# Performance work log

Measured on AMD Instinct MI355X. Metric: run time of the kernel, lower is better.

The kernel has to match this reference:

```python
import jax, jax.numpy as jnp
import numpy as np

NEAR, FAR, N_SAMPLES = 0.5, 2.5, 64


def setup_inputs() -> dict:
    key = jax.random.key(0)
    ks = jax.random.split(key, 12)
    N = 4096
    W = 256  # MLP width
    inp = {
        "rays_o": jax.random.normal(ks[0], (N, 3), jnp.float32),
        "rays_d": jax.random.normal(ks[1], (N, 3), jnp.float32),
        "t_rand": jax.random.uniform(ks[2], (N, N_SAMPLES), jnp.float32),
        "W1": jax.random.normal(ks[3], (3, W), jnp.float32) * 0.5,
        "b1": jnp.zeros((W,), jnp.float32),
        "W2": jax.random.normal(ks[4], (W, W), jnp.float32) * (1.0 / np.sqrt(W)),
        "b2": jnp.zeros((W,), jnp.float32),
        "W3": jax.random.normal(ks[5], (W, W), jnp.float32) * (1.0 / np.sqrt(W)),
        "b3": jnp.zeros((W,), jnp.float32),
        "Wd": jax.random.normal(ks[6], (W, 1), jnp.float32) * (1.0 / np.sqrt(W)),
        "bd": jnp.zeros((1,), jnp.float32),
        "W4": jax.random.normal(ks[7], (W + 3, 128), jnp.float32) * (1.0 / np.sqrt(W + 3)),
        "b4": jnp.zeros((128,), jnp.float32),
        "W5": jax.random.normal(ks[8], (128, 3), jnp.float32) * (1.0 / np.sqrt(128)),
        "b5": jnp.zeros((3,), jnp.float32),
    }
    return inp


def _nerf_mlp(pts, viewdirs, W1, b1, W2, b2, W3, b3, Wd, bd, W4, b4, W5, b5):
    # pts, viewdirs: [N, S, 3] -> rgb [N, S, 3], density [N, S]
    h = jax.nn.relu(pts @ W1 + b1)
    h = jax.nn.relu(h @ W2 + b2)
    h = jax.nn.relu(h @ W3 + b3)
    density = (h @ Wd + bd)[..., 0]
    h2 = jax.nn.relu(jnp.concatenate([h, viewdirs], axis=-1) @ W4 + b4)
    rgb = jax.nn.sigmoid(h2 @ W5 + b5)
    return rgb, density


def reference(rays_o, rays_d, t_rand, W1, b1, W2, b2, W3, b3, Wd, bd, W4, b4, W5, b5):
    N = rays_o.shape[0]
    # Stratified sampling along rays
    t_vals = jnp.linspace(0.0, 1.0, N_SAMPLES, dtype=jnp.float32)
    z = NEAR * (1.0 - t_vals) + FAR * t_vals                      # [S]
    z_vals = jnp.broadcast_to(z, (N, N_SAMPLES))
    mids = 0.5 * (z_vals[:, 1:] + z_vals[:, :-1])
    upper = jnp.concatenate([mids, z_vals[:, -1:]], axis=-1)
    lower = jnp.concatenate([z_vals[:, :1], mids], axis=-1)
    z_vals = lower + (upper - lower) * t_rand                      # [N, S]

    pts = rays_o[:, None, :] + rays_d[:, None, :] * z_vals[..., None]  # [N, S, 3]
    viewdirs = rays_d / (jnp.linalg.norm(rays_d, axis=-1, keepdims=True) + 1e-8)
    vdirs = jnp.broadcast_to(viewdirs[:, None, :], pts.shape)

    rgb, density = _nerf_mlp(pts, vdirs, W1, b1, W2, b2, W3, b3, Wd, bd, W4, b4, W5, b5)

    # Alpha compositing
    dists = z_vals[:, 1:] - z_vals[:, :-1]
    dists = jnp.concatenate([dists, jnp.full_like(dists[:, :1], 1e10)], axis=-1)
    alpha = 1.0 - jnp.exp(-jax.nn.relu(density) * dists)           # [N, S]
    trans = jnp.cumprod(
        jnp.concatenate([jnp.ones_like(alpha[:, :1]), 1.0 - alpha[:, :-1] + 1e-10], axis=-1),
        axis=-1,
    )
    weights = alpha * trans                                        # [N, S]
    rgb_map = jnp.sum(weights[..., None] * rgb, axis=-2)           # [N, 3]
    depth_map = jnp.sum(weights * z_vals, axis=-1)                 # [N]
    acc_map = jnp.sum(weights, axis=-1)                            # [N]
    rgb_map = rgb_map + (1.0 - acc_map[..., None])  # white background
    return rgb_map, depth_map, acc_map
```

## Files before the change

kernel.cpp:

```cpp
#include <hip/hip_runtime.h>
#include <stdint.h>


#define NRAYS 4096

typedef unsigned short u16;
typedef __attribute__((ext_vector_type(8))) short short8;
typedef __attribute__((ext_vector_type(4))) float f32x4;
typedef __attribute__((ext_vector_type(4))) unsigned int uint32x4;

__device__ __forceinline__ u16 f2bf(float f) {
  union { float f; uint32_t i; } v; v.f = f;
  return (u16)((v.i + 0x7FFFu + ((v.i >> 16) & 1u)) >> 16);
}
__device__ __forceinline__ float bf2f(u16 u) {
  union { uint32_t i; float f; } v; v.i = ((uint32_t)u) << 16; return v.f;
}
__device__ __forceinline__ uint32_t cvtpk(float lo, float hi) {
  uint32_t r;
  asm("v_cvt_pk_bf16_f32 %0, %1, %2" : "=v"(r) : "v"(lo), "v"(hi));
  return r;
}

__device__ __forceinline__ int fragidx(int n, int k) {
  return ((((n >> 4) * 8 + (k >> 5)) * 64 + ((k >> 3) & 3) * 16 + (n & 15)) << 3) + (k & 7);
}

__global__ void pack_weights(const float* __restrict__ W2, const float* __restrict__ W3,
                             const float* __restrict__ W4, const float* __restrict__ Wd,
                             const float* __restrict__ W5, u16* __restrict__ ws) {
  int idx = blockIdx.x * 256 + threadIdx.x;
  float v;
  int dst;
  if (idx < 65536) {
    int k = idx >> 8, n = idx & 255;
    v = W2[idx];
    dst = fragidx(n, k);
  } else if (idx < 131072) {
    int o = idx - 65536, k = o >> 8, n = o & 255;
    v = W3[o];
    dst = 65536 + fragidx(n, k);
  } else if (idx < 163840) {
    int o = idx - 131072, k = o >> 7, n = o & 127;
    v = W4[o];
    dst = 131072 + fragidx(n, k);
  } else if (idx < 167936) {
    int o = idx - 163840, k = o >> 4, n = o & 15;
    v = (n == 0) ? Wd[k] : 0.f;
    dst = 163840 + fragidx(n, k);
  } else {
    int o = idx - 167936, k = o >> 4, n = o & 15;
    v = (n < 3) ? W5[k * 3 + n] : 0.f;
    dst = 167936 + fragidx(n, k);
  }
  ws[dst] = f2bf(v);
}

#define MFMA __builtin_amdgcn_mfma_f32_16x16x32_bf16
#define ZER4 (f32x4){0.f, 0.f, 0.f, 0.f}

#define LDA4(ACT, SQ)                                                          \
    short8 av0 = *(const short8*)((ACT) + m0 * 256 + (((SQ) ^ (m0 & 31)) << 3)); \
    short8 av1 = *(const short8*)((ACT) + m1 * 256 + (((SQ) ^ (m1 & 31)) << 3)); \
    short8 av2 = *(const short8*)((ACT) + m2 * 256 + (((SQ) ^ (m2 & 31)) << 3)); \
    short8 av3 = *(const short8*)((ACT) + m3 * 256 + (((SQ) ^ (m3 & 31)) << 3))

#define MF16v(B0, B1, B2_, B3_) do {                                         \
    c00 = MFMA(av0, B0, c00, 0, 0, 0); c10 = MFMA(av1, B0, c10, 0, 0, 0);    \
    c20 = MFMA(av2, B0, c20, 0, 0, 0); c30 = MFMA(av3, B0, c30, 0, 0, 0);    \
    c01 = MFMA(av0, B1, c01, 0, 0, 0); c11 = MFMA(av1, B1, c11, 0, 0, 0);    \
    c21 = MFMA(av2, B1, c21, 0, 0, 0); c31 = MFMA(av3, B1, c31, 0, 0, 0);    \
    c02 = MFMA(av0, B2_, c02, 0, 0, 0); c12 = MFMA(av1, B2_, c12, 0, 0, 0);  \
    c22 = MFMA(av2, B2_, c22, 0, 0, 0); c32 = MFMA(av3, B2_, c32, 0, 0, 0);  \
    c03 = MFMA(av0, B3_, c03, 0, 0, 0); c13 = MFMA(av1, B3_, c13, 0, 0, 0);  \
    c23 = MFMA(av2, B3_, c23, 0, 0, 0); c33 = MFMA(av3, B3_, c33, 0, 0, 0);  \
  } while (0)

#define EPIC(CV, mt, ng, addv, ACT) do {                                     \
    int su_ = ((ng) >> 3), so_ = ((ng) & 7);                                 \
    float f0_ = fmaxf((CV)[0] + (addv), 0.f);                                \
    float f1_ = fmaxf((CV)[1] + (addv), 0.f);                                \
    float f2_ = fmaxf((CV)[2] + (addv), 0.f);                                \
    float f3_ = fmaxf((CV)[3] + (addv), 0.f);                                \
    uint32_t p01_ = cvtpk(f0_, f1_), p23_ = cvtpk(f2_, f3_);                 \
    int mmb_ = (mt) * 16 + quad * 4;                                         \
    (ACT)[(mmb_ + 0) * 256 + ((su_ ^ ((mmb_ + 0) & 31)) << 3) + so_] = (u16)p01_;         \
    (ACT)[(mmb_ + 1) * 256 + ((su_ ^ ((mmb_ + 1) & 31)) << 3) + so_] = (u16)(p01_ >> 16); \
    (ACT)[(mmb_ + 2) * 256 + ((su_ ^ ((mmb_ + 2) & 31)) << 3) + so_] = (u16)p23_;         \
    (ACT)[(mmb_ + 3) * 256 + ((su_ ^ ((mmb_ + 3) & 31)) << 3) + so_] = (u16)(p23_ >> 16); \
  } while (0)

__global__ void __launch_bounds__(256, 2) nerf_fused(
    const float* __restrict__ rays_o, const float* __restrict__ rays_d,
    const float* __restrict__ t_rand,
    const float* __restrict__ W1, const float* __restrict__ b1,
    const float* __restrict__ b2, const float* __restrict__ b3,
    const float* __restrict__ bd,
    const float* __restrict__ W4, const float* __restrict__ b4,
    const float* __restrict__ b5,
    const u16* __restrict__ wpack, float* __restrict__ out) {
  __shared__ u16   actA[64 * 256];
  __shared__ u16   actB[64 * 256];
  __shared__ float w1L[1040];
  __shared__ float zv[64];
  __shared__ float dist[64];
  __shared__ float dens[64];
  __shared__ float rgbL[64 * 4];
  __shared__ float vdirL[4];
  __shared__ float b5L[4];

  const int t = threadIdx.x;
  const int lane = t & 63;
  const int wv = t >> 6;
  const int quad = lane >> 4;
  const int l15 = lane & 15;
  const int ray = blockIdx.x;
  const int m0 = l15, m1 = l15 + 16, m2 = l15 + 32, m3 = l15 + 48;

  short8 B2a[8], B2b[8], B2c[8], B2d[8];
  {
    const u16* q0 = wpack + (wv * 4 + 0) * 4096 + lane * 8;
    const u16* q1 = wpack + (wv * 4 + 1) * 4096 + lane * 8;
    const u16* q2 = wpack + (wv * 4 + 2) * 4096 + lane * 8;
    const u16* q3 = wpack + (wv * 4 + 3) * 4096 + lane * 8;
#pragma unroll
    for (int kq = 0; kq < 8; kq++) {
      B2a[kq] = *(const short8*)(q0 + kq * 512);
      B2b[kq] = *(const short8*)(q1 + kq * 512);
      B2c[kq] = *(const short8*)(q2 + kq * 512);
      B2d[kq] = *(const short8*)(q3 + kq * 512);
    }
  }

  if (t < 64) {
    int j = t;
    float fj = (float)j;
    float zj = 0.5f + 2.0f * (fj / 63.0f);
    float lower = (j == 0)  ? zj : 0.5f * (zj + (0.5f + 2.0f * ((fj - 1.0f) / 63.0f)));
    float upper = (j == 63) ? zj : 0.5f * (zj + (0.5f + 2.0f * ((fj + 1.0f) / 63.0f)));
    float tr = t_rand[ray * 64 + j];
    zv[j] = lower + (upper - lower) * tr;
  }
  {
    int base = (t + (t >> 6)) * 4;
    w1L[base + 0] = W1[t];
    w1L[base + 1] = W1[256 + t];
    w1L[base + 2] = W1[512 + t];
    w1L[base + 3] = b1[t];
  }
  if (t < 3) b5L[t] = b5[t];
  if (t == 3) b5L[3] = bd[0];
  if (t == 0) {
    float dx = rays_d[ray * 3 + 0];
    float dy = rays_d[ray * 3 + 1];
    float dz = rays_d[ray * 3 + 2];
    float nrm = sqrtf(dx * dx + dy * dy + dz * dz) + 1e-8f;
    vdirL[0] = dx / nrm; vdirL[1] = dy / nrm; vdirL[2] = dz / nrm;
  }
  __syncthreads();

  if (t < 64) dist[t] = (t < 63) ? (zv[t + 1] - zv[t]) : 1e10f;

  {
    int m = t >> 2, p = t & 3;
    float zm = zv[m];
    float px = rays_o[ray * 3 + 0] + rays_d[ray * 3 + 0] * zm;
    float py = rays_o[ray * 3 + 1] + rays_d[ray * 3 + 1] * zm;
    float pz = rays_o[ray * 3 + 2] + rays_d[ray * 3 + 2] * zm;
#pragma unroll 1
    for (int kk = 0; kk < 64; kk += 8) {
      float r[8];
#pragma unroll
      for (int j = 0; j < 8; j++) {
        int k = p * 64 + kk + j;
        f32x4 w = *(const f32x4*)(w1L + (k + p) * 4);
        r[j] = fmaxf(w[3] + px * w[0] + py * w[1] + pz * w[2], 0.f);
      }
      uint32x4 pk;
      pk[0] = cvtpk(r[0], r[1]);
      pk[1] = cvtpk(r[2], r[3]);
      pk[2] = cvtpk(r[4], r[5]);
      pk[3] = cvtpk(r[6], r[7]);
      int k0 = p * 64 + kk;
      int u = (k0 >> 3) ^ (m & 31);
      *(uint32x4*)(actA + m * 256 + u * 8) = pk;
    }
  }
  __syncthreads();

  short8 B3a[4], B3b[4], B3c[4], B3d[4];

  {
    int ng0 = wv * 64 + l15;
    float bi0 = b2[ng0], bi1 = b2[ng0 + 16], bi2 = b2[ng0 + 32], bi3 = b2[ng0 + 48];
    f32x4 c00 = ZER4, c01 = ZER4, c02 = ZER4, c03 = ZER4;
    f32x4 c10 = ZER4, c11 = ZER4, c12 = ZER4, c13 = ZER4;
    f32x4 c20 = ZER4, c21 = ZER4, c22 = ZER4, c23 = ZER4;
    f32x4 c30 = ZER4, c31 = ZER4, c32 = ZER4, c33 = ZER4;
#pragma unroll
    for (int kq = 0; kq < 8; kq++) {
      LDA4(actA, kq * 4 + quad);
      MF16v(B2a[kq], B2b[kq], B2c[kq], B2d[kq]);
    }
    {
      const u16* r0 = wpack + 65536 + (wv * 4 + 0) * 4096 + lane * 8;
      const u16* r1 = wpack + 65536 + (wv * 4 + 1) * 4096 + lane * 8;
      const u16* r2 = wpack + 65536 + (wv * 4 + 2) * 4096 + lane * 8;
      const u16* r3 = wpack + 65536 + (wv * 4 + 3) * 4096 + lane * 8;
#pragma unroll
      for (int kq = 0; kq < 4; kq++) {
        B3a[kq] = *(const short8*)(r0 + kq * 512);
        B3b[kq] = *(const short8*)(r1 + kq * 512);
        B3c[kq] = *(const short8*)(r2 + kq * 512);
        B3d[kq] = *(const short8*)(r3 + kq * 512);
      }
    }
    EPIC(c00, 0, ng0, bi0, actB); EPIC(c10, 1, ng0, bi0, actB);
    EPIC(c20, 2, ng0, bi0, actB); EPIC(c30, 3, ng0, bi0, actB);
    EPIC(c01, 0, ng0 + 16, bi1, actB); EPIC(c11, 1, ng0 + 16, bi1, actB);
    EPIC(c21, 2, ng0 + 16, bi1, actB); EPIC(c31, 3, ng0 + 16, bi1, actB);
    EPIC(c02, 0, ng0 + 32, bi2, actB); EPIC(c12, 1, ng0 + 32, bi2, actB);
    EPIC(c22, 2, ng0 + 32, bi2, actB); EPIC(c32, 3, ng0 + 32, bi2, actB);
    EPIC(c03, 0, ng0 + 48, bi3, actB); EPIC(c13, 1, ng0 + 48, bi3, actB);
    EPIC(c23, 2, ng0 + 48, bi3, actB); EPIC(c33, 3, ng0 + 48, bi3, actB);
  }
  __syncthreads();

  short8 L4a[2], L4b[2], L4d[2];

  {
    int ng0 = wv * 64 + l15;
    float bi0 = b3[ng0], bi1 = b3[ng0 + 16], bi2 = b3[ng0 + 32], bi3 = b3[ng0 + 48];
    const u16* r0 = wpack + 65536 + (wv * 4 + 0) * 4096 + lane * 8;
    const u16* r1 = wpack + 65536 + (wv * 4 + 1) * 4096 + lane * 8;
    const u16* r2 = wpack + 65536 + (wv * 4 + 2) * 4096 + lane * 8;
    const u16* r3 = wpack + 65536 + (wv * 4 + 3) * 4096 + lane * 8;
    f32x4 c00 = ZER4, c01 = ZER4, c02 = ZER4, c03 = ZER4;
    f32x4 c10 = ZER4, c11 = ZER4, c12 = ZER4, c13 = ZER4;
    f32x4 c20 = ZER4, c21 = ZER4, c22 = ZER4, c23 = ZER4;
    f32x4 c30 = ZER4, c31 = ZER4, c32 = ZER4, c33 = ZER4;
#pragma unroll
    for (int kq = 0; kq < 8; kq++) {
      short8 b0, b1v, b2v, b3v;
      if (kq < 4) { b0 = B3a[kq]; b1v = B3b[kq]; b2v = B3c[kq]; b3v = B3d[kq]; }
      else {
        b0 = *(const short8*)(r0 + kq * 512);
        b1v = *(const short8*)(r1 + kq * 512);
        b2v = *(const short8*)(r2 + kq * 512);
        b3v = *(const short8*)(r3 + kq * 512);
      }
      LDA4(actB, kq * 4 + quad);
      MF16v(b0, b1v, b2v, b3v);
    }
    {
      const u16* s0 = wpack + 131072 + (wv * 2 + 0) * 4096 + lane * 8;
      const u16* s1 = wpack + 131072 + (wv * 2 + 1) * 4096 + lane * 8;
      const u16* sD = wpack + 163840 + lane * 8;
#pragma unroll
      for (int kq = 0; kq < 2; kq++) {
        L4a[kq] = *(const short8*)(s0 + kq * 512);
        L4b[kq] = *(const short8*)(s1 + kq * 512);
        L4d[kq] = *(const short8*)(sD + kq * 512);
      }
    }
    EPIC(c00, 0, ng0, bi0, actA); EPIC(c10, 1, ng0, bi0, actA);
    EPIC(c20, 2, ng0, bi0, actA); EPIC(c30, 3, ng0, bi0, actA);
    EPIC(c01, 0, ng0 + 16, bi1, actA); EPIC(c11, 1, ng0 + 16, bi1, actA);
    EPIC(c21, 2, ng0 + 16, bi1, actA); EPIC(c31, 3, ng0 + 16, bi1, actA);
    EPIC(c02, 0, ng0 + 32, bi2, actA); EPIC(c12, 1, ng0 + 32, bi2, actA);
    EPIC(c22, 2, ng0 + 32, bi2, actA); EPIC(c32, 3, ng0 + 32, bi2, actA);
    EPIC(c03, 0, ng0 + 48, bi3, actA); EPIC(c13, 1, ng0 + 48, bi3, actA);
    EPIC(c23, 2, ng0 + 48, bi3, actA); EPIC(c33, 3, ng0 + 48, bi3, actA);
  }
  __syncthreads();

  short8 W5f[4];

  {
    float v0 = vdirL[0], v1 = vdirL[1], v2 = vdirL[2];
    int ng0 = wv * 32 + l15;
    int ng1 = ng0 + 16;
    float ad0 = b4[ng0] + v0 * W4[32768 + ng0] + v1 * W4[32896 + ng0] + v2 * W4[33024 + ng0];
    float ad1 = b4[ng1] + v0 * W4[32768 + ng1] + v1 * W4[32896 + ng1] + v2 * W4[33024 + ng1];
    const u16* s0 = wpack + 131072 + (wv * 2 + 0) * 4096 + lane * 8;
    const u16* s1 = wpack + 131072 + (wv * 2 + 1) * 4096 + lane * 8;
    const u16* sD = wpack + 163840 + lane * 8;
    f32x4 c00 = ZER4, c01 = ZER4;
    f32x4 c10 = ZER4, c11 = ZER4;
    f32x4 c20 = ZER4, c21 = ZER4;
    f32x4 c30 = ZER4, c31 = ZER4;
    f32x4 c40 = ZER4, c41 = ZER4, c42 = ZER4, c43 = ZER4;
#pragma unroll
    for (int kq = 0; kq < 8; kq++) {
      short8 b0 = (kq < 2) ? L4a[kq] : *(const short8*)(s0 + kq * 512);
      short8 b1v = (kq < 2) ? L4b[kq] : *(const short8*)(s1 + kq * 512);
      short8 bD = (kq < 2) ? L4d[kq] : *(const short8*)(sD + kq * 512);
      LDA4(actA, kq * 4 + quad);
      c00 = MFMA(av0, b0, c00, 0, 0, 0); c10 = MFMA(av1, b0, c10, 0, 0, 0);
      c20 = MFMA(av2, b0, c20, 0, 0, 0); c30 = MFMA(av3, b0, c30, 0, 0, 0);
      c01 = MFMA(av0, b1v, c01, 0, 0, 0); c11 = MFMA(av1, b1v, c11, 0, 0, 0);
      c21 = MFMA(av2, b1v, c21, 0, 0, 0); c31 = MFMA(av3, b1v, c31, 0, 0, 0);
      c40 = MFMA(av0, bD, c40, 0, 0, 0); c41 = MFMA(av1, bD, c41, 0, 0, 0);
      c42 = MFMA(av2, bD, c42, 0, 0, 0); c43 = MFMA(av3, bD, c43, 0, 0, 0);
    }
    {
      const u16* s5 = wpack + 167936 + lane * 8;
#pragma unroll
      for (int kq = 0; kq < 4; kq++) W5f[kq] = *(const short8*)(s5 + kq * 512);
    }
    EPIC(c00, 0, ng0, ad0, actB); EPIC(c10, 1, ng0, ad0, actB);
    EPIC(c20, 2, ng0, ad0, actB); EPIC(c30, 3, ng0, ad0, actB);
    EPIC(c01, 0, ng1, ad1, actB); EPIC(c11, 1, ng1, ad1, actB);
    EPIC(c21, 2, ng1, ad1, actB); EPIC(c31, 3, ng1, ad1, actB);
    if (wv == 0 && l15 == 0) {
#pragma unroll
      for (int r = 0; r < 4; r++) {
        dens[ 0 + quad * 4 + r] = c40[r];
        dens[16 + quad * 4 + r] = c41[r];
        dens[32 + quad * 4 + r] = c42[r];
        dens[48 + quad * 4 + r] = c43[r];
      }
    }
  }
  __syncthreads();

  {
    int mR = wv * 16 + l15;
    f32x4 cR = ZER4;
#pragma unroll
    for (int kq = 0; kq < 4; kq++) {
      short8 av = *(const short8*)(actB + mR * 256 + (((kq * 4 + quad) ^ (mR & 31)) << 3));
      cR = MFMA(av, W5f[kq], cR, 0, 0, 0);
    }
    if (l15 < 3) {
#pragma unroll
      for (int r = 0; r < 4; r++) {
        int row = wv * 16 + quad * 4 + r;
        rgbL[row * 4 + l15] = 1.f / (1.f + __expf(-(cR[r] + b5L[l15])));
      }
    }
  }
  __syncthreads();

  if (t < 64) {
    int j = t;
    float alpha = 1.f - __expf(-fmaxf(dens[j] + b5L[3], 0.f) * dist[j]);
    float v = 1.f - alpha + 1e-10f;
    float pscan = v;
#pragma unroll
    for (int d = 1; d < 64; d <<= 1) {
      float o = __shfl_up(pscan, d);
      if (j >= d) pscan *= o;
    }
    float T = __shfl_up(pscan, 1);
    if (j == 0) T = 1.f;
    float w = alpha * T;
    float r0 = w * rgbL[j * 4 + 0];
    float r1 = w * rgbL[j * 4 + 1];
    float r2 = w * rgbL[j * 4 + 2];
    float dp = w * zv[j];
    float ac = w;
#pragma unroll
    for (int d = 32; d; d >>= 1) {
      r0 += __shfl_down(r0, d);
      r1 += __shfl_down(r1, d);
      r2 += __shfl_down(r2, d);
      dp += __shfl_down(dp, d);
      ac += __shfl_down(ac, d);
    }
    if (j == 0) {
      float bg = 1.f - ac;
      out[ray * 3 + 0] = r0 + bg;
      out[ray * 3 + 1] = r1 + bg;
      out[ray * 3 + 2] = r2 + bg;
      out[NRAYS * 3 + ray] = dp;
      out[NRAYS * 4 + ray] = ac;
    }
  }
}

extern "C" void kernel_launch(void* const* d_in, const int* in_sizes, int n_in,
                              void* d_out, int out_size, void* d_ws, size_t ws_size,
                              hipStream_t stream) {
  const float* rays_o = (const float*)d_in[0];
  const float* rays_d = (const float*)d_in[1];
  const float* t_rand = (const float*)d_in[2];
  const float* W1 = (const float*)d_in[3];
  const float* b1 = (const float*)d_in[4];
  const float* W2 = (const float*)d_in[5];
  const float* b2 = (const float*)d_in[6];
  const float* W3 = (const float*)d_in[7];
  const float* b3 = (const float*)d_in[8];
  const float* Wd = (const float*)d_in[9];
  const float* bd = (const float*)d_in[10];
  const float* W4 = (const float*)d_in[11];
  const float* b4 = (const float*)d_in[12];
  const float* W5 = (const float*)d_in[13];
  const float* b5 = (const float*)d_in[14];
  u16* wpack = (u16*)d_ws;
  float* out = (float*)d_out;

  pack_weights<<<664, 256, 0, stream>>>(W2, W3, W4, Wd, W5, wpack);
  nerf_fused<<<NRAYS, 256, 0, stream>>>(rays_o, rays_d, t_rand, W1, b1, b2, b3,
                                        bd, W4, b4, b5, wpack, out);
}
```

Measured before the change: 216.9 us.

## Compute first MLP layer with MFMA using split-bf16 inputs and remove a barrier

The first layer (3->256 plus bias) now runs on MFMA instead of scalar FMAs from LDS. Each point coordinate is split into a bf16 high part and a bf16 low part so the result stays accurate, and the bias is folded in through a constant-one column of pre-packed W1. This removes the w1L/zv/dist shared-memory setup and one __syncthreads. The W2 register prefetch is split around the first-layer MFMAs, and more W3 fragments are kept in registers. The final rgb MFMA and compositing now run in wave 0 only, with z values recomputed by shuffles, which trades register pressure and a serial tail for fewer barriers.

```diff
diff --git a/kernel.cpp b/kernel.cpp
--- a/kernel.cpp
+++ b/kernel.cpp
@@ -7,7 +7,6 @@
 typedef unsigned short u16;
 typedef __attribute__((ext_vector_type(8))) short short8;
 typedef __attribute__((ext_vector_type(4))) float f32x4;
-typedef __attribute__((ext_vector_type(4))) unsigned int uint32x4;
 
 __device__ __forceinline__ u16 f2bf(float f) {
   union { float f; uint32_t i; } v; v.f = f;
@@ -22,11 +21,23 @@
   return r;
 }
 
+__device__ __forceinline__ float zval(int j, float tr) {
+  float fj = (float)j;
+  float zj = 0.5f + 2.0f * (fj / 63.0f);
+  float lower = (j == 0)  ? zj : 0.5f * (zj + (0.5f + 2.0f * ((fj - 1.0f) / 63.0f)));
+  float upper = (j == 63) ? zj : 0.5f * (zj + (0.5f + 2.0f * ((fj + 1.0f) / 63.0f)));
+  return lower + (upper - lower) * tr;
+}
+
 __device__ __forceinline__ int fragidx(int n, int k) {
   return ((((n >> 4) * 8 + (k >> 5)) * 64 + ((k >> 3) & 3) * 16 + (n & 15)) << 3) + (k & 7);
 }
-
-__global__ void pack_weights(const float* __restrict__ W2, const float* __restrict__ W3,
+__device__ __forceinline__ int fragidx32(int n, int k) {
+  return (((n >> 4) * 64 + ((k >> 3) & 3) * 16 + (n & 15)) << 3) + (k & 7);
+}
+
+__global__ void pack_weights(const float* __restrict__ W1, const float* __restrict__ b1,
+                             const float* __restrict__ W2, const float* __restrict__ W3,
                              const float* __restrict__ W4, const float* __restrict__ Wd,
                              const float* __restrict__ W5, u16* __restrict__ ws) {
   int idx = blockIdx.x * 256 + threadIdx.x;
@@ -48,10 +59,16 @@
     int o = idx - 163840, k = o >> 4, n = o & 15;
     v = (n == 0) ? Wd[k] : 0.f;
     dst = 163840 + fragidx(n, k);
-  } else {
+  } else if (idx < 169984) {
     int o = idx - 167936, k = o >> 4, n = o & 15;
     v = (n < 3) ? W5[k * 3 + n] : 0.f;
     dst = 167936 + fragidx(n, k);
+  } else {
+    int o = idx - 169984, k = o >> 8, n = o & 255;
+    if (k < 6)      v = W1[(k >> 1) * 256 + n];
+    else if (k == 6) v = b1[n];
+    else            v = 0.f;
+    dst = 169984 + fragidx32(n, k);
   }
   ws[dst] = f2bf(v);
 }
@@ -93,7 +110,6 @@
 __global__ void __launch_bounds__(256, 2) nerf_fused(
     const float* __restrict__ rays_o, const float* __restrict__ rays_d,
     const float* __restrict__ t_rand,
-    const float* __restrict__ W1, const float* __restrict__ b1,
     const float* __restrict__ b2, const float* __restrict__ b3,
     const float* __restrict__ bd,
     const float* __restrict__ W4, const float* __restrict__ b4,
@@ -101,13 +117,8 @@
     const u16* __restrict__ wpack, float* __restrict__ out) {
   __shared__ u16   actA[64 * 256];
   __shared__ u16   actB[64 * 256];
-  __shared__ float w1L[1040];
-  __shared__ float zv[64];
-  __shared__ float dist[64];
   __shared__ float dens[64];
   __shared__ float rgbL[64 * 4];
-  __shared__ float vdirL[4];
-  __shared__ float b5L[4];
 
   const int t = threadIdx.x;
   const int lane = t & 63;
@@ -117,78 +128,77 @@
   const int ray = blockIdx.x;
   const int m0 = l15, m1 = l15 + 16, m2 = l15 + 32, m3 = l15 + 48;
 
+  short8 W1f0, W1f1, W1f2, W1f3;
+  {
+    const u16* w1b = wpack + 169984 + (wv * 4) * 512 + lane * 8;
+    W1f0 = *(const short8*)(w1b);
+    W1f1 = *(const short8*)(w1b + 512);
+    W1f2 = *(const short8*)(w1b + 1024);
+    W1f3 = *(const short8*)(w1b + 1536);
+  }
   short8 B2a[8], B2b[8], B2c[8], B2d[8];
+  const u16* q0 = wpack + (wv * 4 + 0) * 4096 + lane * 8;
+  const u16* q1 = wpack + (wv * 4 + 1) * 4096 + lane * 8;
+  const u16* q2 = wpack + (wv * 4 + 2) * 4096 + lane * 8;
+  const u16* q3 = wpack + (wv * 4 + 3) * 4096 + lane * 8;
+#pragma unroll
+  for (int kq = 0; kq < 4; kq++) {
+    B2a[kq] = *(const short8*)(q0 + kq * 512);
+    B2b[kq] = *(const short8*)(q1 + kq * 512);
+    B2c[kq] = *(const short8*)(q2 + kq * 512);
+    B2d[kq] = *(const short8*)(q3 + kq * 512);
+  }
+
+  const float rox = rays_o[ray * 3 + 0], roy = rays_o[ray * 3 + 1], roz = rays_o[ray * 3 + 2];
+  const float rdx = rays_d[ray * 3 + 0], rdy = rays_d[ray * 3 + 1], rdz = rays_d[ray * 3 + 2];
+
   {
-    const u16* q0 = wpack + (wv * 4 + 0) * 4096 + lane * 8;
-    const u16* q1 = wpack + (wv * 4 + 1) * 4096 + lane * 8;
-    const u16* q2 = wpack + (wv * 4 + 2) * 4096 + lane * 8;
-    const u16* q3 = wpack + (wv * 4 + 3) * 4096 + lane * 8;
-#pragma unroll
-    for (int kq = 0; kq < 8; kq++) {
+    short8 avz = {0, 0, 0, 0, 0, 0, 0, 0};
+    short8 av0 = avz, av1 = avz, av2 = avz, av3 = avz;
+    if (quad == 0) {
+#pragma unroll
+      for (int r = 0; r < 4; r++) {
+        int m = l15 + r * 16;
+        float tr = t_rand[ray * 64 + m];
+        float zm = zval(m, tr);
+        float px = rox + rdx * zm, py = roy + rdy * zm, pz = roz + rdz * zm;
+        u16 xh = f2bf(px); float xl = px - bf2f(xh);
+        u16 yh = f2bf(py); float yl = py - bf2f(yh);
+        u16 zh = f2bf(pz); float zl = pz - bf2f(zh);
+        short8 f;
+        f[0] = (short)xh; f[1] = (short)f2bf(xl);
+        f[2] = (short)yh; f[3] = (short)f2bf(yl);
+        f[4] = (short)zh; f[5] = (short)f2bf(zl);
+        f[6] = (short)0x3F80; f[7] = 0;
+        if (r == 0) av0 = f; else if (r == 1) av1 = f;
+        else if (r == 2) av2 = f; else av3 = f;
+      }
+    }
+    f32x4 c00 = ZER4, c01 = ZER4, c02 = ZER4, c03 = ZER4;
+    f32x4 c10 = ZER4, c11 = ZER4, c12 = ZER4, c13 = ZER4;
+    f32x4 c20 = ZER4, c21 = ZER4, c22 = ZER4, c23 = ZER4;
+    f32x4 c30 = ZER4, c31 = ZER4, c32 = ZER4, c33 = ZER4;
+    MF16v(W1f0, W1f1, W1f2, W1f3);
+#pragma unroll
+    for (int kq = 4; kq < 8; kq++) {
       B2a[kq] = *(const short8*)(q0 + kq * 512);
       B2b[kq] = *(const short8*)(q1 + kq * 512);
       B2c[kq] = *(const short8*)(q2 + kq * 512);
       B2d[kq] = *(const short8*)(q3 + kq * 512);
     }
-  }
-
-  if (t < 64) {
-    int j = t;
-    float fj = (float)j;
-    float zj = 0.5f + 2.0f * (fj / 63.0f);
-    float lower = (j == 0)  ? zj : 0.5f * (zj + (0.5f + 2.0f * ((fj - 1.0f) / 63.0f)));
-    float upper = (j == 63) ? zj : 0.5f * (zj + (0.5f + 2.0f * ((fj + 1.0f) / 63.0f)));
-    float tr = t_rand[ray * 64 + j];
-    zv[j] = lower + (upper - lower) * tr;
-  }
-  {
-    int base = (t + (t >> 6)) * 4;
-    w1L[base + 0] = W1[t];
-    w1L[base + 1] = W1[256 + t];
-    w1L[base + 2] = W1[512 + t];
-    w1L[base + 3] = b1[t];
-  }
-  if (t < 3) b5L[t] = b5[t];
-  if (t == 3) b5L[3] = bd[0];
-  if (t == 0) {
-    float dx = rays_d[ray * 3 + 0];
-    float dy = rays_d[ray * 3 + 1];
-    float dz = rays_d[ray * 3 + 2];
-    float nrm = sqrtf(dx * dx + dy * dy + dz * dz) + 1e-8f;
-    vdirL[0] = dx / nrm; vdirL[1] = dy / nrm; vdirL[2] = dz / nrm;
+    int ng0 = wv * 64 + l15;
+    EPIC(c00, 0, ng0, 0.f, actA); EPIC(c10, 1, ng0, 0.f, actA);
+    EPIC(c20, 2, ng0, 0.f, actA); EPIC(c30, 3, ng0, 0.f, actA);
+    EPIC(c01, 0, ng0 + 16, 0.f, actA); EPIC(c11, 1, ng0 + 16, 0.f, actA);
+    EPIC(c21, 2, ng0 + 16, 0.f, actA); EPIC(c31, 3, ng0 + 16, 0.f, actA);
+    EPIC(c02, 0, ng0 + 32, 0.f, actA); EPIC(c12, 1, ng0 + 32, 0.f, actA);
+    EPIC(c22, 2, ng0 + 32, 0.f, actA); EPIC(c32, 3, ng0 + 32, 0.f, actA);
+    EPIC(c03, 0, ng0 + 48, 0.f, actA); EPIC(c13, 1, ng0 + 48, 0.f, actA);
+    EPIC(c23, 2, ng0 + 48, 0.f, actA); EPIC(c33, 3, ng0 + 48, 0.f, actA);
   }
   __syncthreads();
 
-  if (t < 64) dist[t] = (t < 63) ? (zv[t + 1] - zv[t]) : 1e10f;
-
-  {
-    int m = t >> 2, p = t & 3;
-    float zm = zv[m];
-    float px = rays_o[ray * 3 + 0] + rays_d[ray * 3 + 0] * zm;
-    float py = rays_o[ray * 3 + 1] + rays_d[ray * 3 + 1] * zm;
-    float pz = rays_o[ray * 3 + 2] + rays_d[ray * 3 + 2] * zm;
-#pragma unroll 1
-    for (int kk = 0; kk < 64; kk += 8) {
-      float r[8];
-#pragma unroll
-      for (int j = 0; j < 8; j++) {
-        int k = p * 64 + kk + j;
-        f32x4 w = *(const f32x4*)(w1L + (k + p) * 4);
-        r[j] = fmaxf(w[3] + px * w[0] + py * w[1] + pz * w[2], 0.f);
-      }
-      uint32x4 pk;
-      pk[0] = cvtpk(r[0], r[1]);
-      pk[1] = cvtpk(r[2], r[3]);
-      pk[2] = cvtpk(r[4], r[5]);
-      pk[3] = cvtpk(r[6], r[7]);
-      int k0 = p * 64 + kk;
-      int u = (k0 >> 3) ^ (m & 31);
-      *(uint32x4*)(actA + m * 256 + u * 8) = pk;
-    }
-  }
-  __syncthreads();
-
-  short8 B3a[4], B3b[4], B3c[4], B3d[4];
+  short8 B3a[6], B3b[6], B3c[6], B3d[6];
 
   {
     int ng0 = wv * 64 + l15;
@@ -208,7 +218,7 @@
       const u16* r2 = wpack + 65536 + (wv * 4 + 2) * 4096 + lane * 8;
       const u16* r3 = wpack + 65536 + (wv * 4 + 3) * 4096 + lane * 8;
 #pragma unroll
-      for (int kq = 0; kq < 4; kq++) {
+      for (int kq = 0; kq < 6; kq++) {
         B3a[kq] = *(const short8*)(r0 + kq * 512);
         B3b[kq] = *(const short8*)(r1 + kq * 512);
         B3c[kq] = *(const short8*)(r2 + kq * 512);
@@ -242,7 +252,7 @@
 #pragma unroll
     for (int kq = 0; kq < 8; kq++) {
       short8 b0, b1v, b2v, b3v;
-      if (kq < 4) { b0 = B3a[kq]; b1v = B3b[kq]; b2v = B3c[kq]; b3v = B3d[kq]; }
+      if (kq < 6) { b0 = B3a[kq]; b1v = B3b[kq]; b2v = B3c[kq]; b3v = B3d[kq]; }
       else {
         b0 = *(const short8*)(r0 + kq * 512);
         b1v = *(const short8*)(r1 + kq * 512);
@@ -277,7 +287,8 @@
   short8 W5f[4];
 
   {
-    float v0 = vdirL[0], v1 = vdirL[1], v2 = vdirL[2];
+    float nrm = sqrtf(rdx * rdx + rdy * rdy + rdz * rdz) + 1e-8f;
+    float v0 = rdx / nrm, v1 = rdy / nrm, v2 = rdz / nrm;
     int ng0 = wv * 32 + l15;
     int ng1 = ng0 + 16;
     float ad0 = b4[ng0] + v0 * W4[32768 + ng0] + v1 * W4[32896 + ng0] + v2 * W4[33024 + ng0];
@@ -303,7 +314,7 @@
       c40 = MFMA(av0, bD, c40, 0, 0, 0); c41 = MFMA(av1, bD, c41, 0, 0, 0);
       c42 = MFMA(av2, bD, c42, 0, 0, 0); c43 = MFMA(av3, bD, c43, 0, 0, 0);
     }
-    {
+    if (wv == 0) {
       const u16* s5 = wpack + 167936 + lane * 8;
 #pragma unroll
       for (int kq = 0; kq < 4; kq++) W5f[kq] = *(const short8*)(s5 + kq * 512);
@@ -324,57 +335,67 @@
   }
   __syncthreads();
 
-  {
-    int mR = wv * 16 + l15;
-    f32x4 cR = ZER4;
-#pragma unroll
-    for (int kq = 0; kq < 4; kq++) {
-      short8 av = *(const short8*)(actB + mR * 256 + (((kq * 4 + quad) ^ (mR & 31)) << 3));
-      cR = MFMA(av, W5f[kq], cR, 0, 0, 0);
-    }
-    if (l15 < 3) {
-#pragma unroll
-      for (int r = 0; r < 4; r++) {
-        int row = wv * 16 + quad * 4 + r;
-        rgbL[row * 4 + l15] = 1.f / (1.f + __expf(-(cR[r] + b5L[l15])));
-      }
-    }
-  }
-  __syncthreads();
-
-  if (t < 64) {
-    int j = t;
-    float alpha = 1.f - __expf(-fmaxf(dens[j] + b5L[3], 0.f) * dist[j]);
-    float v = 1.f - alpha + 1e-10f;
-    float pscan = v;
-#pragma unroll
-    for (int d = 1; d < 64; d <<= 1) {
-      float o = __shfl_up(pscan, d);
-      if (j >= d) pscan *= o;
-    }
-    float T = __shfl_up(pscan, 1);
-    if (j == 0) T = 1.f;
-    float w = alpha * T;
-    float r0 = w * rgbL[j * 4 + 0];
-    float r1 = w * rgbL[j * 4 + 1];
-    float r2 = w * rgbL[j * 4 + 2];
-    float dp = w * zv[j];
-    float ac = w;
-#pragma unroll
-    for (int d = 32; d; d >>= 1) {
-      r0 += __shfl_down(r0, d);
-      r1 += __shfl_down(r1, d);
-      r2 += __shfl_down(r2, d);
-      dp += __shfl_down(dp, d);
-      ac += __shfl_down(ac, d);
-    }
-    if (j == 0) {
-      float bg = 1.f - ac;
-      out[ray * 3 + 0] = r0 + bg;
-      out[ray * 3 + 1] = r1 + bg;
-      out[ray * 3 + 2] = r2 + bg;
-      out[NRAYS * 3 + ray] = dp;
-      out[NRAYS * 4 + ray] = ac;
+  if (wv == 0) {
+    {
+      f32x4 cR0 = ZER4, cR1 = ZER4, cR2 = ZER4, cR3 = ZER4;
+#pragma unroll
+      for (int kq = 0; kq < 4; kq++) {
+        LDA4(actB, kq * 4 + quad);
+        cR0 = MFMA(av0, W5f[kq], cR0, 0, 0, 0);
+        cR1 = MFMA(av1, W5f[kq], cR1, 0, 0, 0);
+        cR2 = MFMA(av2, W5f[kq], cR2, 0, 0, 0);
+        cR3 = MFMA(av3, W5f[kq], cR3, 0, 0, 0);
+      }
+      if (l15 < 3) {
+        float b5v = b5[l15];
+#pragma unroll
+        for (int r = 0; r < 4; r++) {
+          rgbL[( 0 + quad * 4 + r) * 4 + l15] = 1.f / (1.f + __expf(-(cR0[r] + b5v)));
+          rgbL[(16 + quad * 4 + r) * 4 + l15] = 1.f / (1.f + __expf(-(cR1[r] + b5v)));
+          rgbL[(32 + quad * 4 + r) * 4 + l15] = 1.f / (1.f + __expf(-(cR2[r] + b5v)));
+          rgbL[(48 + quad * 4 + r) * 4 + l15] = 1.f / (1.f + __expf(-(cR3[r] + b5v)));
+        }
+      }
+    }
+    {
+      int j = lane;
+      float tr = t_rand[ray * 64 + j];
+      float zvj = zval(j, tr);
+      float zvn = __shfl_down(zvj, 1);
+      float dist = (j < 63) ? (zvn - zvj) : 1e10f;
+      float bd0 = bd[0];
+      float alpha = 1.f - __expf(-fmaxf(dens[j] + bd0, 0.f) * dist);
+      float v = 1.f - alpha + 1e-10f;
+      float pscan = v;
+#pragma unroll
+      for (int d = 1; d < 64; d <<= 1) {
+        float o = __shfl_up(pscan, d);
+        if (j >= d) pscan *= o;
+      }
+      float T = __shfl_up(pscan, 1);
+      if (j == 0) T = 1.f;
+      float w = alpha * T;
+      float r0 = w * rgbL[j * 4 + 0];
+      float r1 = w * rgbL[j * 4 + 1];
+      float r2 = w * rgbL[j * 4 + 2];
+      float dp = w * zvj;
+      float ac = w;
+#pragma unroll
+      for (int d = 32; d; d >>= 1) {
+        r0 += __shfl_down(r0, d);
+        r1 += __shfl_down(r1, d);
+        r2 += __shfl_down(r2, d);
+        dp += __shfl_down(dp, d);
+        ac += __shfl_down(ac, d);
+      }
+      if (j == 0) {
+        float bg = 1.f - ac;
+        out[ray * 3 + 0] = r0 + bg;
+        out[ray * 3 + 1] = r1 + bg;
+        out[ray * 3 + 2] = r2 + bg;
+        out[NRAYS * 3 + ray] = dp;
+        out[NRAYS * 4 + ray] = ac;
+      }
     }
   }
 }
@@ -400,7 +421,7 @@
   u16* wpack = (u16*)d_ws;
   float* out = (float*)d_out;
 
-  pack_weights<<<664, 256, 0, stream>>>(W2, W3, W4, Wd, W5, wpack);
-  nerf_fused<<<NRAYS, 256, 0, stream>>>(rays_o, rays_d, t_rand, W1, b1, b2, b3,
+  pack_weights<<<696, 256, 0, stream>>>(W1, b1, W2, W3, W4, Wd, W5, wpack);
+  nerf_fused<<<NRAYS, 256, 0, stream>>>(rays_o, rays_d, t_rand, b2, b3,
                                         bd, W4, b4, b5, wpack, out);
 }
```

Measured after the change: 373.3 us. 1.72x slower.
